# Performance work log

Hardware: AMD Instinct MI355X
Metric: run time of the kernel (lower is better)

The kernel has to match this reference:

```python
import jax, jax.numpy as jnp
import numpy as np

K = 5      # kernel_size
STRIDE = 1
EPS = 1e-7


def _extract_patches(x, k, s):
    # x: [B,H,W,C] -> [B,Ho,Wo,k,k,C], same (kh,kw,c) layout as tf.extract_image_patches VALID
    B, H, W, C = x.shape
    Ho = (H - k) // s + 1
    Wo = (W - k) // s + 1
    r = (jnp.arange(Ho) * s)[:, None] + jnp.arange(k)   # [Ho,k]
    c = (jnp.arange(Wo) * s)[:, None] + jnp.arange(k)   # [Wo,k]
    return x[:, r[:, None, :, None], c[None, :, None, :], :]


def _rotate(pflat, angle, k):
    # Replicates tf.contrib.image.transform with angles_to_projective_transforms,
    # including the (1+1e-7) normalization of the 3x3 matrix in the original code.
    # pflat: [N, k*k, C], angle: [N]; bilinear sampling, fill value 0 outside.
    N = pflat.shape[0]
    f32 = pflat.dtype
    co, si = jnp.cos(angle), jnp.sin(angle)
    km1 = jnp.asarray(k - 1, f32)
    xoff = (km1 - (co * km1 - si * km1)) * 0.5
    yoff = (km1 - (si * km1 + co * km1)) * 0.5
    scale = 1.0 / (1.0 + EPS)  # transforms /= transforms[:, 8:9] + 1e-7
    gy, gx = jnp.meshgrid(jnp.arange(k, dtype=f32), jnp.arange(k, dtype=f32), indexing='ij')
    sx = (co[:, None, None] * gx - si[:, None, None] * gy + xoff[:, None, None]) * scale
    sy = (si[:, None, None] * gx + co[:, None, None] * gy + yoff[:, None, None]) * scale
    sx = sx.reshape(N, k * k)
    sy = sy.reshape(N, k * k)
    x0 = jnp.floor(sx)
    y0 = jnp.floor(sy)
    wx = (sx - x0)[..., None]
    wy = (sy - y0)[..., None]
    x0i = x0.astype(jnp.int32)
    y0i = y0.astype(jnp.int32)

    def samp(yi, xi):
        valid = (xi >= 0) & (xi < k) & (yi >= 0) & (yi < k)
        idx = jnp.clip(yi, 0, k - 1) * k + jnp.clip(xi, 0, k - 1)   # [N,k*k]
        v = jnp.take_along_axis(pflat, idx[..., None], axis=1)      # [N,k*k,C]
        return jnp.where(valid[..., None], v, jnp.zeros((), f32))

    v00 = samp(y0i, x0i)
    v01 = samp(y0i, x0i + 1)
    v10 = samp(y0i + 1, x0i)
    v11 = samp(y0i + 1, x0i + 1)
    top = v00 * (1 - wx) + v01 * wx
    bot = v10 * (1 - wx) + v11 * wx
    return top * (1 - wy) + bot * wy   # [N,k*k,C]


def _forward(input_tensor, W, b):
    k, s = K, STRIDE
    B, H, Wd, C = input_tensor.shape
    patches = _extract_patches(input_tensor, k, s)      # [B,Ho,Wo,k,k,C]
    Ho, Wo = patches.shape[1], patches.shape[2]
    inten = patches.sum(-1)                             # [B,Ho,Wo,k,k] channel-sum intensity
    ridx = jnp.arange(k, dtype=patches.dtype)
    tot = inten.sum((-2, -1)) + EPS
    cr = (inten * ridx[:, None]).sum((-2, -1)) / tot    # centroid row
    cc = (inten * ridx[None, :]).sum((-2, -1)) / tot    # centroid col
    m = (k - 1) / 2.0                                   # meanCenter (same for row/col)
    angle = jnp.arctan2(cr - m, cc - m + EPS)           # [B,Ho,Wo]
    pflat = patches.reshape(B * Ho * Wo, k * k, C)
    rot = _rotate(pflat, angle.reshape(-1), k)          # [N,k*k,C]
    rot = rot.reshape(B, Ho * Wo, k * k * C)
    wflat = W.reshape(W.shape[0], -1)                   # [F, k*k*C]
    out = jnp.einsum('bpd,fd->bpf', rot, wflat)         # elementwise-mult-sum 'conv'
    return out.reshape(B, Ho, Wo, -1) + b


def setup_inputs():
    key = jax.random.key(0)
    k1, k2 = jax.random.split(key, 2)
    B, H, Wd, C, F = 4, 128, 128, 16, 32
    input_tensor = jax.random.uniform(k1, (B, H, Wd, C), dtype=jnp.float32)
    lim = float(np.sqrt(6.0 / (K * K * C + F)))  # glorot_uniform
    W = jax.random.uniform(k2, (F, K, K, C), minval=-lim, maxval=lim, dtype=jnp.float32)
    b = jnp.zeros((F,), jnp.float32)
    return {"input_tensor": input_tensor, "W": W, "b": b}


def reference(input_tensor, W, b):
    return _forward(input_tensor, W, b)
```

## Files before the change

kernel.cpp:

```cpp
#include <hip/hip_runtime.h>


#define KS     5
#define TILE   8
#define TW     (TILE + KS - 1)
#define CPAD   20
#define C_IN   16
#define F_OUT  32
#define H_IN   128
#define W_IN   128
#define HO     124
#define WO     124
#define NBATCH 4
#define EPSF   1e-7f
#define BLOCK  256
#define NTAP   25
#define KW     400

typedef __attribute__((ext_vector_type(8)))  short short8;
typedef __attribute__((ext_vector_type(16))) float floatx16;

static __device__ __forceinline__ unsigned f2bfu(float f) {
    union { float f; unsigned u; } v; v.f = f;
    unsigned r = v.u + 0x7fffu + ((v.u >> 16) & 1u);
    return r >> 16;
}
static __device__ __forceinline__ unsigned pack2(float a, float b) {
    return f2bfu(a) | (f2bfu(b) << 16);
}

__global__ __launch_bounds__(BLOCK, 4) void rotconv_kernel(
    const float* __restrict__ in, const float* __restrict__ Wg,
    const float* __restrict__ bg, float* __restrict__ out)
{
    __shared__ float s_in[TW * TW * CPAD];
    __shared__ float s_int[TW * (TW + 1)];
    __shared__ union {
        short w[NTAP * 64 * 8];
        float red[3 * 2048];
    } uW;

    const int tid  = threadIdx.x;
    const int bx = blockIdx.x, by = blockIdx.y, bimg = blockIdx.z;
    const int ox = bx * TILE, oy = by * TILE;
    const int p  = tid & 63;
    const int wv = __builtin_amdgcn_readfirstlane(tid >> 6);
    const int lx = p & 7, ly = p >> 3;

    for (int i = tid; i < NTAP * 64; i += BLOCK) {
        int t = i >> 6, l = i & 63;
        const float* wp = Wg + (size_t)(l & 31) * KW + t * 16 + (l >> 5) * 8;
        float4 a = *(const float4*)(wp);
        float4 b = *(const float4*)(wp + 4);
        unsigned* d = (unsigned*)&uW.w[i * 8];
        d[0] = pack2(a.x, a.y); d[1] = pack2(a.z, a.w);
        d[2] = pack2(b.x, b.y); d[3] = pack2(b.z, b.w);
    }

    const float* inb = in + (size_t)bimg * (H_IN * W_IN * C_IN);
    for (int i = tid; i < TW * TW * (C_IN / 4); i += BLOCK) {
        int cv = i & 3;
        int pp = i >> 2;
        int x = pp % TW, y = pp / TW;
        int gy = oy + y, gx = ox + x;
        float4 v = make_float4(0.f, 0.f, 0.f, 0.f);
        if (gy < H_IN && gx < W_IN)
            v = *(const float4*)(inb + ((size_t)(gy * W_IN + gx) * C_IN) + 4 * cv);
        *(float4*)(&s_in[pp * CPAD + 4 * cv]) = v;
    }
    __syncthreads();

    for (int pp = tid; pp < TW * TW; pp += BLOCK) {
        const float* sp = &s_in[pp * CPAD];
        float s = 0.f;
        #pragma unroll
        for (int c = 0; c < C_IN; ++c) s += sp[c];
        s_int[(pp / TW) * (TW + 1) + (pp % TW)] = s;
    }
    __syncthreads();

    float tot = EPSF, cr = 0.f, cc = 0.f;
    #pragma unroll
    for (int dy = 0; dy < KS; ++dy)
        #pragma unroll
        for (int dx = 0; dx < KS; ++dx) {
            float v = s_int[(ly + dy) * (TW + 1) + (lx + dx)];
            tot += v; cr += v * (float)dy; cc += v * (float)dx;
        }
    cr /= tot; cc /= tot;
    float ang = atan2f(cr - 2.0f, cc - 2.0f + EPSF);
    float si, co;
    sincosf(ang, &si, &co);
    const float scl = 1.0f / (1.0f + EPSF);
    float xoff = (4.0f - (co * 4.0f - si * 4.0f)) * 0.5f;
    float yoff = (4.0f - (si * 4.0f + co * 4.0f)) * 0.5f;

    floatx16 acc0 = {0}, acc1 = {0};

    for (int i = 0; i < 7; ++i) {
        int t = wv + 4 * i;
        if (t < NTAP) {
            int ky = t / KS, kx = t - KS * ky;
            float sx = (co * (float)kx - si * (float)ky + xoff) * scl;
            float sy = (si * (float)kx + co * (float)ky + yoff) * scl;
            float fx0 = floorf(sx), fy0 = floorf(sy);
            float wx = sx - fx0, wy = sy - fy0;
            int x0 = (int)fx0, y0 = (int)fy0;
            int x1 = x0 + 1, y1 = y0 + 1;
            float vx0 = (x0 >= 0 && x0 < KS) ? 1.f : 0.f;
            float vx1 = (x1 >= 0 && x1 < KS) ? 1.f : 0.f;
            float vy0 = (y0 >= 0 && y0 < KS) ? 1.f : 0.f;
            float vy1 = (y1 >= 0 && y1 < KS) ? 1.f : 0.f;
            float w00 = (1.f - wx) * (1.f - wy) * vx0 * vy0;
            float w01 = wx * (1.f - wy) * vx1 * vy0;
            float w10 = (1.f - wx) * wy * vx0 * vy1;
            float w11 = wx * wy * vx1 * vy1;
            int cx0 = min(max(x0, 0), KS - 1), cx1 = min(max(x1, 0), KS - 1);
            int cy0 = min(max(y0, 0), KS - 1), cy1 = min(max(y1, 0), KS - 1);
            const float* p00 = &s_in[((ly + cy0) * TW + (lx + cx0)) * CPAD];
            const float* p01 = &s_in[((ly + cy0) * TW + (lx + cx1)) * CPAD];
            const float* p10 = &s_in[((ly + cy1) * TW + (lx + cx0)) * CPAD];
            const float* p11 = &s_in[((ly + cy1) * TW + (lx + cx1)) * CPAD];
            float r[16];
            #pragma unroll
            for (int cv = 0; cv < 4; ++cv) {
                float4 a = *(const float4*)(p00 + 4 * cv);
                float4 b = *(const float4*)(p01 + 4 * cv);
                float4 c = *(const float4*)(p10 + 4 * cv);
                float4 d = *(const float4*)(p11 + 4 * cv);
                r[4*cv+0] = w00 * a.x + w01 * b.x + w10 * c.x + w11 * d.x;
                r[4*cv+1] = w00 * a.y + w01 * b.y + w10 * c.y + w11 * d.y;
                r[4*cv+2] = w00 * a.z + w01 * b.z + w10 * c.z + w11 * d.z;
                r[4*cv+3] = w00 * a.w + w01 * b.w + w10 * c.w + w11 * d.w;
            }
            unsigned lo[4], hi[4];
            #pragma unroll
            for (int d = 0; d < 4; ++d) {
                lo[d] = pack2(r[2*d],     r[2*d + 1]);
                hi[d] = pack2(r[8 + 2*d], r[9 + 2*d]);
            }
            union { unsigned u[4]; short8 v; } a0, a1;
            #pragma unroll
            for (int d = 0; d < 4; ++d) {
                unsigned snd = (p < 32) ? hi[d] : lo[d];
                unsigned rcv = (unsigned)__shfl((int)snd, p ^ 32, 64);
                a0.u[d] = (p < 32) ? lo[d] : rcv;
                a1.u[d] = (p < 32) ? rcv : hi[d];
            }
            short8 bf = *(const short8*)(&uW.w[(t * 64 + p) * 8]);
            acc0 = __builtin_amdgcn_mfma_f32_32x32x16_bf16(a0.v, bf, acc0, 0, 0, 0);
            acc1 = __builtin_amdgcn_mfma_f32_32x32x16_bf16(a1.v, bf, acc1, 0, 0, 0);
        }
    }

    __syncthreads();
    if (wv > 0) {
        float* red = &uW.red[(wv - 1) * 2048];
        #pragma unroll
        for (int r = 0; r < 16; ++r) {
            red[r * 64 + p]         = acc0[r];
            red[(16 + r) * 64 + p]  = acc1[r];
        }
    }
    __syncthreads();

    if (wv == 0) {
        float bias = bg[p & 31];
        #pragma unroll
        for (int T = 0; T < 2; ++T) {
            #pragma unroll
            for (int r = 0; r < 16; ++r) {
                int s = T * 16 + r;
                float v = (T == 0 ? acc0[r] : acc1[r])
                        + uW.red[s * 64 + p]
                        + uW.red[2048 + s * 64 + p]
                        + uW.red[4096 + s * 64 + p] + bias;
                int px = T * 32 + (r & 3) + 8 * (r >> 2) + 4 * (p >> 5);
                int ho = oy + (px >> 3), wo = ox + (px & 7);
                if (ho < HO && wo < WO)
                    out[(((size_t)bimg * HO + ho) * WO + wo) * F_OUT + (p & 31)] = v;
            }
        }
    }
}

extern "C" void kernel_launch(void* const* d_in, const int* in_sizes, int n_in,
                              void* d_out, int out_size, void* d_ws, size_t ws_size,
                              hipStream_t stream) {
    const float* in = (const float*)d_in[0];
    const float* Wg = (const float*)d_in[1];
    const float* bg = (const float*)d_in[2];
    float* out      = (float*)d_out;
    dim3 grid((WO + TILE - 1) / TILE, (HO + TILE - 1) / TILE, NBATCH);
    rotconv_kernel<<<grid, dim3(BLOCK), 0, stream>>>(in, Wg, bg, out);
}
```

Before: 80.88 us.

## Split pixel tiles across wave pairs, drop shuffles, fuse load and intensity sum

After: 77.06 us. -4.7%, faster.

```diff
diff --git a/kernel.cpp b/kernel.cpp
--- a/kernel.cpp
+++ b/kernel.cpp
@@ -37,15 +37,20 @@
     __shared__ float s_int[TW * (TW + 1)];
     __shared__ union {
         short w[NTAP * 64 * 8];
-        float red[3 * 2048];
+        float red[2 * 1024];
     } uW;
 
-    const int tid  = threadIdx.x;
+    const int tid = threadIdx.x;
     const int bx = blockIdx.x, by = blockIdx.y, bimg = blockIdx.z;
     const int ox = bx * TILE, oy = by * TILE;
     const int p  = tid & 63;
     const int wv = __builtin_amdgcn_readfirstlane(tid >> 6);
-    const int lx = p & 7, ly = p >> 3;
+    const int tile = wv >> 1;
+    const int par  = wv & 1;
+    const int m32  = p & 31;
+    const int half = p >> 5;
+    const int q    = tile * 32 + m32;
+    const int lx = q & 7, ly = q >> 3;
 
     for (int i = tid; i < NTAP * 64; i += BLOCK) {
         int t = i >> 6, l = i & 63;
@@ -58,24 +63,21 @@
     }
 
     const float* inb = in + (size_t)bimg * (H_IN * W_IN * C_IN);
-    for (int i = tid; i < TW * TW * (C_IN / 4); i += BLOCK) {
-        int cv = i & 3;
-        int pp = i >> 2;
-        int x = pp % TW, y = pp / TW;
+    if (tid < TW * TW) {
+        int x = tid % TW, y = tid / TW;
         int gy = oy + y, gx = ox + x;
-        float4 v = make_float4(0.f, 0.f, 0.f, 0.f);
-        if (gy < H_IN && gx < W_IN)
-            v = *(const float4*)(inb + ((size_t)(gy * W_IN + gx) * C_IN) + 4 * cv);
-        *(float4*)(&s_in[pp * CPAD + 4 * cv]) = v;
-    }
-    __syncthreads();
-
-    for (int pp = tid; pp < TW * TW; pp += BLOCK) {
-        const float* sp = &s_in[pp * CPAD];
-        float s = 0.f;
-        #pragma unroll
-        for (int c = 0; c < C_IN; ++c) s += sp[c];
-        s_int[(pp / TW) * (TW + 1) + (pp % TW)] = s;
+        float4 v0 = {0,0,0,0}, v1 = {0,0,0,0}, v2 = {0,0,0,0}, v3 = {0,0,0,0};
+        if (gy < H_IN && gx < W_IN) {
+            const float* g = inb + (size_t)(gy * W_IN + gx) * C_IN;
+            v0 = *(const float4*)(g);      v1 = *(const float4*)(g + 4);
+            v2 = *(const float4*)(g + 8);  v3 = *(const float4*)(g + 12);
+        }
+        float* d = &s_in[tid * CPAD];
+        *(float4*)(d)      = v0; *(float4*)(d + 4)  = v1;
+        *(float4*)(d + 8)  = v2; *(float4*)(d + 12) = v3;
+        s_int[y * (TW + 1) + x] =
+            (v0.x+v0.y+v0.z+v0.w) + (v1.x+v1.y+v1.z+v1.w) +
+            (v2.x+v2.y+v2.z+v2.w) + (v3.x+v3.y+v3.z+v3.w);
     }
     __syncthreads();
 
@@ -88,98 +90,76 @@
             tot += v; cr += v * (float)dy; cc += v * (float)dx;
         }
     cr /= tot; cc /= tot;
-    float ang = atan2f(cr - 2.0f, cc - 2.0f + EPSF);
-    float si, co;
-    sincosf(ang, &si, &co);
+    float yv = cr - 2.0f;
+    float xv = cc - 2.0f + EPSF;
+    float rh = rsqrtf(fmaxf(xv * xv + yv * yv, 1e-30f));
+    float co = xv * rh, si = yv * rh;
     const float scl = 1.0f / (1.0f + EPSF);
     float xoff = (4.0f - (co * 4.0f - si * 4.0f)) * 0.5f;
     float yoff = (4.0f - (si * 4.0f + co * 4.0f)) * 0.5f;
 
-    floatx16 acc0 = {0}, acc1 = {0};
+    floatx16 acc = {0};
 
-    for (int i = 0; i < 7; ++i) {
-        int t = wv + 4 * i;
-        if (t < NTAP) {
-            int ky = t / KS, kx = t - KS * ky;
-            float sx = (co * (float)kx - si * (float)ky + xoff) * scl;
-            float sy = (si * (float)kx + co * (float)ky + yoff) * scl;
-            float fx0 = floorf(sx), fy0 = floorf(sy);
-            float wx = sx - fx0, wy = sy - fy0;
-            int x0 = (int)fx0, y0 = (int)fy0;
-            int x1 = x0 + 1, y1 = y0 + 1;
-            float vx0 = (x0 >= 0 && x0 < KS) ? 1.f : 0.f;
-            float vx1 = (x1 >= 0 && x1 < KS) ? 1.f : 0.f;
-            float vy0 = (y0 >= 0 && y0 < KS) ? 1.f : 0.f;
-            float vy1 = (y1 >= 0 && y1 < KS) ? 1.f : 0.f;
-            float w00 = (1.f - wx) * (1.f - wy) * vx0 * vy0;
-            float w01 = wx * (1.f - wy) * vx1 * vy0;
-            float w10 = (1.f - wx) * wy * vx0 * vy1;
-            float w11 = wx * wy * vx1 * vy1;
-            int cx0 = min(max(x0, 0), KS - 1), cx1 = min(max(x1, 0), KS - 1);
-            int cy0 = min(max(y0, 0), KS - 1), cy1 = min(max(y1, 0), KS - 1);
-            const float* p00 = &s_in[((ly + cy0) * TW + (lx + cx0)) * CPAD];
-            const float* p01 = &s_in[((ly + cy0) * TW + (lx + cx1)) * CPAD];
-            const float* p10 = &s_in[((ly + cy1) * TW + (lx + cx0)) * CPAD];
-            const float* p11 = &s_in[((ly + cy1) * TW + (lx + cx1)) * CPAD];
-            float r[16];
-            #pragma unroll
-            for (int cv = 0; cv < 4; ++cv) {
-                float4 a = *(const float4*)(p00 + 4 * cv);
-                float4 b = *(const float4*)(p01 + 4 * cv);
-                float4 c = *(const float4*)(p10 + 4 * cv);
-                float4 d = *(const float4*)(p11 + 4 * cv);
-                r[4*cv+0] = w00 * a.x + w01 * b.x + w10 * c.x + w11 * d.x;
-                r[4*cv+1] = w00 * a.y + w01 * b.y + w10 * c.y + w11 * d.y;
-                r[4*cv+2] = w00 * a.z + w01 * b.z + w10 * c.z + w11 * d.z;
-                r[4*cv+3] = w00 * a.w + w01 * b.w + w10 * c.w + w11 * d.w;
-            }
-            unsigned lo[4], hi[4];
-            #pragma unroll
-            for (int d = 0; d < 4; ++d) {
-                lo[d] = pack2(r[2*d],     r[2*d + 1]);
-                hi[d] = pack2(r[8 + 2*d], r[9 + 2*d]);
-            }
-            union { unsigned u[4]; short8 v; } a0, a1;
-            #pragma unroll
-            for (int d = 0; d < 4; ++d) {
-                unsigned snd = (p < 32) ? hi[d] : lo[d];
-                unsigned rcv = (unsigned)__shfl((int)snd, p ^ 32, 64);
-                a0.u[d] = (p < 32) ? lo[d] : rcv;
-                a1.u[d] = (p < 32) ? rcv : hi[d];
-            }
-            short8 bf = *(const short8*)(&uW.w[(t * 64 + p) * 8]);
-            acc0 = __builtin_amdgcn_mfma_f32_32x32x16_bf16(a0.v, bf, acc0, 0, 0, 0);
-            acc1 = __builtin_amdgcn_mfma_f32_32x32x16_bf16(a1.v, bf, acc1, 0, 0, 0);
-        }
+    for (int i = 0; i < 13; ++i) {
+        int t = 2 * i + par;
+        float live = (t < NTAP) ? 1.f : 0.f;
+        int tt = min(t, NTAP - 1);
+        int ky = tt / KS, kx = tt - KS * ky;
+        float sx = (co * (float)kx - si * (float)ky + xoff) * scl;
+        float sy = (si * (float)kx + co * (float)ky + yoff) * scl;
+        float fx0 = floorf(sx), fy0 = floorf(sy);
+        float wx = sx - fx0, wy = sy - fy0;
+        int x0 = (int)fx0, y0 = (int)fy0;
+        int x1 = x0 + 1, y1 = y0 + 1;
+        float vx0 = (x0 >= 0 && x0 < KS) ? live : 0.f;
+        float vx1 = (x1 >= 0 && x1 < KS) ? live : 0.f;
+        float vy0 = (y0 >= 0 && y0 < KS) ? 1.f : 0.f;
+        float vy1 = (y1 >= 0 && y1 < KS) ? 1.f : 0.f;
+        float w00 = (1.f - wx) * (1.f - wy) * vx0 * vy0;
+        float w01 = wx * (1.f - wy) * vx1 * vy0;
+        float w10 = (1.f - wx) * wy * vx0 * vy1;
+        float w11 = wx * wy * vx1 * vy1;
+        int cx0 = min(max(x0, 0), KS - 1), cx1 = min(max(x1, 0), KS - 1);
+        int cy0 = min(max(y0, 0), KS - 1), cy1 = min(max(y1, 0), KS - 1);
+        const float* p00 = &s_in[((ly + cy0) * TW + (lx + cx0)) * CPAD + half * 8];
+        const float* p01 = &s_in[((ly + cy0) * TW + (lx + cx1)) * CPAD + half * 8];
+        const float* p10 = &s_in[((ly + cy1) * TW + (lx + cx0)) * CPAD + half * 8];
+        const float* p11 = &s_in[((ly + cy1) * TW + (lx + cx1)) * CPAD + half * 8];
+        float4 a0 = *(const float4*)(p00), a1 = *(const float4*)(p00 + 4);
+        float4 b0 = *(const float4*)(p01), b1 = *(const float4*)(p01 + 4);
+        float4 c0 = *(const float4*)(p10), c1 = *(const float4*)(p10 + 4);
+        float4 d0 = *(const float4*)(p11), d1 = *(const float4*)(p11 + 4);
+        float r0 = w00*a0.x + w01*b0.x + w10*c0.x + w11*d0.x;
+        float r1 = w00*a0.y + w01*b0.y + w10*c0.y + w11*d0.y;
+        float r2 = w00*a0.z + w01*b0.z + w10*c0.z + w11*d0.z;
+        float r3 = w00*a0.w + w01*b0.w + w10*c0.w + w11*d0.w;
+        float r4 = w00*a1.x + w01*b1.x + w10*c1.x + w11*d1.x;
+        float r5 = w00*a1.y + w01*b1.y + w10*c1.y + w11*d1.y;
+        float r6 = w00*a1.z + w01*b1.z + w10*c1.z + w11*d1.z;
+        float r7 = w00*a1.w + w01*b1.w + w10*c1.w + w11*d1.w;
+        union { unsigned u[4]; short8 v; } af;
+        af.u[0] = pack2(r0, r1); af.u[1] = pack2(r2, r3);
+        af.u[2] = pack2(r4, r5); af.u[3] = pack2(r6, r7);
+        short8 bf = *(const short8*)(&uW.w[(tt * 64 + p) * 8]);
+        acc = __builtin_amdgcn_mfma_f32_32x32x16_bf16(af.v, bf, acc, 0, 0, 0);
     }
 
     __syncthreads();
-    if (wv > 0) {
-        float* red = &uW.red[(wv - 1) * 2048];
+    if (par == 1) {
+        #pragma unroll
+        for (int r = 0; r < 16; ++r)
+            uW.red[tile * 1024 + r * 64 + p] = acc[r];
+    }
+    __syncthreads();
+    if (par == 0) {
+        float bias = bg[p & 31];
         #pragma unroll
         for (int r = 0; r < 16; ++r) {
-            red[r * 64 + p]         = acc0[r];
-            red[(16 + r) * 64 + p]  = acc1[r];
-        }
-    }
-    __syncthreads();
-
-    if (wv == 0) {
-        float bias = bg[p & 31];
-        #pragma unroll
-        for (int T = 0; T < 2; ++T) {
-            #pragma unroll
-            for (int r = 0; r < 16; ++r) {
-                int s = T * 16 + r;
-                float v = (T == 0 ? acc0[r] : acc1[r])
-                        + uW.red[s * 64 + p]
-                        + uW.red[2048 + s * 64 + p]
-                        + uW.red[4096 + s * 64 + p] + bias;
-                int px = T * 32 + (r & 3) + 8 * (r >> 2) + 4 * (p >> 5);
-                int ho = oy + (px >> 3), wo = ox + (px & 7);
-                if (ho < HO && wo < WO)
-                    out[(((size_t)bimg * HO + ho) * WO + wo) * F_OUT + (p & 31)] = v;
-            }
+            float v = acc[r] + uW.red[tile * 1024 + r * 64 + p] + bias;
+            int px = tile * 32 + (r & 3) + 8 * (r >> 2) + 4 * (p >> 5);
+            int ho = oy + (px >> 3), wo = ox + (px & 7);
+            if (ho < HO && wo < WO)
+                out[(((size_t)bimg * HO + ho) * WO + wo) * F_OUT + (p & 31)] = v;
         }
     }
 }
```
